# Performance work log

Hardware: AMD Instinct MI355X
Metric: run time of the kernel (lower is better)

Reference implementation:

```python
import jax, jax.numpy as jnp
import numpy as np

D_MODEL = 1024
NUM_HEADS = 16
DEPTH = D_MODEL // NUM_HEADS


def setup_inputs() -> dict:
    key = jax.random.key(0)
    ks = jax.random.split(key, 9)
    B, S = 2, 2048
    scale = 1.0 / np.sqrt(D_MODEL)
    x = jax.random.normal(ks[0], (B, S, D_MODEL), dtype=jnp.float32)
    wq = jax.random.normal(ks[1], (D_MODEL, D_MODEL), dtype=jnp.float32) * scale
    wk = jax.random.normal(ks[2], (D_MODEL, D_MODEL), dtype=jnp.float32) * scale
    wv = jax.random.normal(ks[3], (D_MODEL, D_MODEL), dtype=jnp.float32) * scale
    wo = jax.random.normal(ks[4], (D_MODEL, D_MODEL), dtype=jnp.float32) * scale
    bq = jnp.zeros((D_MODEL,), dtype=jnp.float32)
    bk = jnp.zeros((D_MODEL,), dtype=jnp.float32)
    bv = jnp.zeros((D_MODEL,), dtype=jnp.float32)
    bo = jnp.zeros((D_MODEL,), dtype=jnp.float32)
    return {"x": x, "wq": wq, "bq": bq, "wk": wk, "bk": bk,
            "wv": wv, "bv": bv, "wo": wo, "bo": bo}


def _split_heads(t):
    # [B, S, D] -> [B, H, S, depth]
    B, S, _ = t.shape
    return t.reshape(B, S, NUM_HEADS, DEPTH).transpose(0, 2, 1, 3)


def reference(x, wq, bq, wk, bk, wv, bv, wo, bo):
    q = _split_heads(x @ wq + bq)
    k = _split_heads(x @ wk + bk)
    v = _split_heads(x @ wv + bv)
    # scaled dot-product attention with materialized [B,H,S,S] scores
    logits = jnp.einsum("bhqd,bhkd->bhqk", q, k) / jnp.sqrt(
        jnp.asarray(DEPTH, dtype=x.dtype))
    attn = jax.nn.softmax(logits, axis=-1)
    out = jnp.einsum("bhqk,bhkd->bhqd", attn, v)
    B, _, S, _ = out.shape
    concat = out.transpose(0, 2, 1, 3).reshape(B, S, D_MODEL)
    return concat @ wo + bo
```

## Files before the change

kernel.cpp:

```cpp
#include <hip/hip_runtime.h>
#include <hip/hip_bf16.h>
#include <stdint.h>

typedef unsigned short u16;
typedef __attribute__((ext_vector_type(8))) short short8;
typedef __attribute__((ext_vector_type(4))) short s4v;
typedef __attribute__((ext_vector_type(4))) float f32x4;

__device__ __forceinline__ float bf2f(u16 u) {
    union { uint32_t u; float f; } v; v.u = ((uint32_t)u) << 16; return v.f;
}
__device__ __forceinline__ u16 f2bf(float f) {
    union { float f; uint32_t u; } v; v.f = f;
    uint32_t r = (v.u + 0x7fffu + ((v.u >> 16) & 1u)) >> 16;
    return (u16)r;
}
__device__ __forceinline__ uint32_t pkbf(float a, float b) {
    union { __hip_bfloat162 h; uint32_t w; } u;
    u.h = __float22bfloat162_rn(float2{a, b});
    return u.w;
}
__device__ __forceinline__ void store_out(u16* p, float v) { *p = f2bf(v); }
__device__ __forceinline__ void store_out(float* p, float v) { *p = v; }

__device__ __forceinline__ void async_ld16(const u16* g, u16* l) {
    __builtin_amdgcn_global_load_lds(
        (const __attribute__((address_space(1))) void*)g,
        (__attribute__((address_space(3))) void*)l, 16, 0, 0);
}

__global__ void cvt_x(const float* __restrict__ x, u16* __restrict__ xb) {
    int i = (blockIdx.x * 256 + threadIdx.x) * 8;
    float4 a = *(const float4*)(x + i);
    float4 b = *(const float4*)(x + i + 4);
    union { uint32_t w[4]; uint4 v; } o;
    o.w[0] = pkbf(a.x, a.y); o.w[1] = pkbf(a.z, a.w);
    o.w[2] = pkbf(b.x, b.y); o.w[3] = pkbf(b.z, b.w);
    *(uint4*)(xb + i) = o.v;
}

__global__ void transpose3(const float* __restrict__ w0, const float* __restrict__ w1,
                           const float* __restrict__ w2, u16* __restrict__ out) {
    const int z = blockIdx.z;
    const float* in = (z == 0) ? w0 : (z == 1) ? w1 : w2;
    u16* o = out + (size_t)z * 1024 * 1024;
    __shared__ u16 tile[32][33];
    int x = blockIdx.x * 32 + threadIdx.x;
    int y0 = blockIdx.y * 32;
#pragma unroll
    for (int j = threadIdx.y; j < 32; j += 8)
        tile[j][threadIdx.x] = f2bf(in[(size_t)(y0 + j) * 1024 + x]);
    __syncthreads();
    int ox = blockIdx.y * 32 + threadIdx.x;
    int oy0 = blockIdx.x * 32;
#pragma unroll
    for (int j = threadIdx.y; j < 32; j += 8)
        o[(size_t)(oy0 + j) * 1024 + ox] = tile[threadIdx.x][j];
}

#define GBM 128
#define GBN 128
#define GBK 32

template <typename OutT>
__global__ __launch_bounds__(256) void gemm_bt(
    const u16* __restrict__ A, int lda,
    const u16* __restrict__ BT, int ldb,
    const float* __restrict__ bias0, const float* __restrict__ bias1,
    const float* __restrict__ bias2,
    OutT* __restrict__ C, int ldc, int K) {
    __shared__ __align__(16) u16 As[GBM * GBK];
    __shared__ __align__(16) u16 Bs[GBN * GBK];

    const int tid = threadIdx.x;
    const int wave = tid >> 6, lane = tid & 63;
    const int quad = lane >> 4, l16 = lane & 15;
    const int wr = wave >> 1, wc = wave & 1;
    const int m0 = blockIdx.y * GBM, n0 = blockIdx.x * GBN;

    const int seg = n0 >> 10;
    const float* bsel = (seg == 0) ? bias0 : (seg == 1) ? bias1 : bias2;

    f32x4 acc[4][4] = {};

    const int srow = tid >> 2;
    const int scol = (tid & 3) * 8;
    const u16* Ag0 = A + (size_t)(m0 + srow) * lda + scol;
    const u16* Ag1 = Ag0 + (size_t)64 * lda;
    const u16* Bg0 = BT + (size_t)(n0 + srow) * ldb + scol;
    const u16* Bg1 = Bg0 + (size_t)64 * ldb;
    u16* As0 = As + (wave << 9);
    u16* As1 = As0 + 64 * GBK;
    u16* Bs0 = Bs + (wave << 9);
    u16* Bs1 = Bs0 + 64 * GBK;

    for (int kb = 0; kb < K; kb += GBK) {
        async_ld16(Ag0 + kb, As0);
        async_ld16(Ag1 + kb, As1);
        async_ld16(Bg0 + kb, Bs0);
        async_ld16(Bg1 + kb, Bs1);
        __syncthreads();

        short8 af[4], bf[4];
#pragma unroll
        for (int mt = 0; mt < 4; mt++)
            af[mt] = *(const short8*)(As + (wr * 64 + mt * 16 + l16) * GBK + quad * 8);
#pragma unroll
        for (int nt = 0; nt < 4; nt++)
            bf[nt] = *(const short8*)(Bs + (wc * 64 + nt * 16 + l16) * GBK + quad * 8);
#pragma unroll
        for (int mt = 0; mt < 4; mt++)
#pragma unroll
            for (int nt = 0; nt < 4; nt++)
                acc[mt][nt] = __builtin_amdgcn_mfma_f32_16x16x32_bf16(
                    af[mt], bf[nt], acc[mt][nt], 0, 0, 0);
        __syncthreads();
    }

#pragma unroll
    for (int nt = 0; nt < 4; nt++) {
        int col = n0 + wc * 64 + nt * 16 + l16;
        float bv = bsel[col & 1023];
#pragma unroll
        for (int mt = 0; mt < 4; mt++) {
            int row = m0 + wr * 64 + mt * 16 + quad * 4;
#pragma unroll
            for (int r = 0; r < 4; r++)
                store_out(&C[(size_t)(row + r) * ldc + col], acc[mt][nt][r] + bv);
        }
    }
}

#define SEQ 2048
#define BQ 64
#define BKV 128
#define LDK 72
#define LDKV 136

__global__ __launch_bounds__(256) void attn(u16* __restrict__ QKV) {
    __shared__ __align__(16) u16 Ks[BKV * LDK];
    __shared__ __align__(16) u16 Vs[64 * LDKV];

    const int tid = threadIdx.x;
    const int wave = tid >> 6, lane = tid & 63;
    const int quad = lane >> 4, l16 = lane & 15;
    const int h = blockIdx.y, bb = blockIdx.z;
    const int q0 = blockIdx.x * BQ;
    const size_t tok0 = (size_t)bb * SEQ;

    const u16* Qb = QKV + tok0 * 3072 + h * 64;
    const u16* Kb = QKV + tok0 * 3072 + 1024 + h * 64;
    const u16* Vb = QKV + tok0 * 3072 + 2048 + h * 64;

    const float cs = 0.18033688011112042f;

    const int qrow = q0 + wave * 16 + l16;
    short8 aq[2];
    {
        union { short8 s; u16 u[8]; uint32_t w[4]; } qa, qb;
        qa.s = *(const short8*)(Qb + (size_t)qrow * 3072 + quad * 8);
        qb.s = *(const short8*)(Qb + (size_t)qrow * 3072 + 32 + quad * 8);
#pragma unroll
        for (int j = 0; j < 4; j++) {
            qa.w[j] = pkbf(bf2f(qa.u[2 * j]) * cs, bf2f(qa.u[2 * j + 1]) * cs);
            qb.w[j] = pkbf(bf2f(qb.u[2 * j]) * cs, bf2f(qb.u[2 * j + 1]) * cs);
        }
        aq[0] = qa.s; aq[1] = qb.s;
    }

    float l_i = 0.0f;
    f32x4 o[4] = {};

    const int srow = tid >> 2;
    const int scc = (tid & 3) * 16;
    const int pr = tid & 63;
    const int dg = wave;

    const u16* kg = Kb + (size_t)srow * 3072 + scc;
    const u16* vg = Vb + (size_t)(2 * pr) * 3072 + dg * 16;

    uint4 k0r = *(const uint4*)(kg);
    uint4 k1r = *(const uint4*)(kg + 8);
    uint4 k2r = *(const uint4*)(kg + (size_t)64 * 3072);
    uint4 k3r = *(const uint4*)(kg + (size_t)64 * 3072 + 8);
    uint4 va0 = *(const uint4*)(vg);
    uint4 va1 = *(const uint4*)(vg + 8);
    uint4 vb0 = *(const uint4*)(vg + 3072);
    uint4 vb1 = *(const uint4*)(vg + 3072 + 8);

    for (int j0 = 0; j0 < SEQ; j0 += BKV) {
        *(uint4*)(Ks + srow * LDK + scc) = k0r;
        *(uint4*)(Ks + srow * LDK + scc + 8) = k1r;
        *(uint4*)(Ks + (srow + 64) * LDK + scc) = k2r;
        *(uint4*)(Ks + (srow + 64) * LDK + scc + 8) = k3r;
        {
            union { uint4 v[2]; u16 u[16]; } a, b;
            a.v[0] = va0; a.v[1] = va1; b.v[0] = vb0; b.v[1] = vb1;
#pragma unroll
            for (int j = 0; j < 16; j++) {
                uint32_t w = (uint32_t)a.u[j] | ((uint32_t)b.u[j] << 16);
                *(uint32_t*)(Vs + (dg * 16 + j) * LDKV + 2 * pr) = w;
            }
        }
        __syncthreads();

        if (j0 + BKV < SEQ) {
            size_t off = (size_t)(j0 + BKV) * 3072;
            k0r = *(const uint4*)(kg + off);
            k1r = *(const uint4*)(kg + off + 8);
            k2r = *(const uint4*)(kg + off + (size_t)64 * 3072);
            k3r = *(const uint4*)(kg + off + (size_t)64 * 3072 + 8);
            va0 = *(const uint4*)(vg + off);
            va1 = *(const uint4*)(vg + off + 8);
            vb0 = *(const uint4*)(vg + off + 3072);
            vb1 = *(const uint4*)(vg + off + 3072 + 8);
        }

        f32x4 st[8];
#pragma unroll
        for (int kkt = 0; kkt < 8; kkt++) {
            f32x4 s = {};
#pragma unroll
            for (int k2 = 0; k2 < 2; k2++) {
                short8 ak = *(const short8*)(Ks + (kkt * 16 + l16) * LDK + k2 * 32 + quad * 8);
                s = __builtin_amdgcn_mfma_f32_16x16x32_bf16(ak, aq[k2], s, 0, 0, 0);
            }
            st[kkt] = s;
        }

#pragma unroll
        for (int kkt = 0; kkt < 8; kkt++)
#pragma unroll
            for (int r = 0; r < 4; r++)
                st[kkt][r] = __builtin_amdgcn_exp2f(st[kkt][r]);

        {
            float ls = 0.0f;
#pragma unroll
            for (int kkt = 0; kkt < 8; kkt++)
#pragma unroll
                for (int r = 0; r < 4; r++) ls += st[kkt][r];
            ls += __shfl_xor(ls, 16, 64);
            ls += __shfl_xor(ls, 32, 64);
            l_i += ls;
        }

#pragma unroll
        for (int kkt = 0; kkt < 8; kkt++) {
            union { uint32_t w[2]; s4v s; } bp;
            bp.w[0] = pkbf(st[kkt][0], st[kkt][1]);
            bp.w[1] = pkbf(st[kkt][2], st[kkt][3]);
#pragma unroll
            for (int dt = 0; dt < 4; dt++) {
                s4v av = *(const s4v*)(Vs + (dt * 16 + l16) * LDKV + kkt * 16 + quad * 4);
                o[dt] = __builtin_amdgcn_mfma_f32_16x16x16bf16_1k(av, bp.s, o[dt], 0, 0, 0);
            }
        }

        __syncthreads();
    }

    const float inv_l = 1.0f / l_i;
    u16* orow = QKV + (tok0 + qrow) * 3072 + h * 64;
#pragma unroll
    for (int dt = 0; dt < 4; dt++) {
        uint32_t w0 = pkbf(o[dt][0] * inv_l, o[dt][1] * inv_l);
        uint32_t w1 = pkbf(o[dt][2] * inv_l, o[dt][3] * inv_l);
        uint2 w = {w0, w1};
        *(uint2*)(orow + dt * 16 + quad * 4) = w;
    }
}

extern "C" void kernel_launch(void* const* d_in, const int* in_sizes, int n_in,
                              void* d_out, int out_size, void* d_ws, size_t ws_size,
                              hipStream_t stream) {
    const float* x  = (const float*)d_in[0];
    const float* wq = (const float*)d_in[1];
    const float* bq = (const float*)d_in[2];
    const float* wk = (const float*)d_in[3];
    const float* bk = (const float*)d_in[4];
    const float* wv = (const float*)d_in[5];
    const float* bv = (const float*)d_in[6];
    const float* wo = (const float*)d_in[7];
    const float* bo = (const float*)d_in[8];
    (void)in_sizes; (void)n_in; (void)out_size; (void)ws_size;

    u16* QKV = (u16*)d_ws;
    u16* wT  = QKV + (size_t)4096 * 3072;
    u16* xb  = wT + (size_t)3 * 1024 * 1024;
    u16* woT = xb;

    cvt_x<<<dim3(2048), dim3(256), 0, stream>>>(x, xb);
    transpose3<<<dim3(32, 32, 3), dim3(32, 8), 0, stream>>>(wq, wk, wv, wT);
    gemm_bt<u16><<<dim3(24, 32), 256, 0, stream>>>(xb, 1024, wT, 1024, bq, bk, bv,
                                                   QKV, 3072, 1024);
    transpose3<<<dim3(32, 32, 1), dim3(32, 8), 0, stream>>>(wo, wo, wo, woT);
    attn<<<dim3(32, 16, 2), 256, 0, stream>>>(QKV);
    gemm_bt<float><<<dim3(8, 32), 256, 0, stream>>>(QKV, 3072, woT, 1024, bo, bo, bo,
                                                    (float*)d_out, 1024, 1024);
}
```

Before: 233.1 us.

## Double query tile per attention block and fold row-sum into MFMA via ones row

```diff
diff --git a/kernel.cpp b/kernel.cpp
--- a/kernel.cpp
+++ b/kernel.cpp
@@ -132,20 +132,20 @@
 }
 
 #define SEQ 2048
-#define BQ 64
+#define BQT 128
 #define BKV 128
 #define LDK 72
 #define LDKV 136
 
-__global__ __launch_bounds__(256) void attn(u16* __restrict__ QKV) {
+__global__ __launch_bounds__(512, 4) void attn(u16* __restrict__ QKV) {
     __shared__ __align__(16) u16 Ks[BKV * LDK];
-    __shared__ __align__(16) u16 Vs[64 * LDKV];
+    __shared__ __align__(16) u16 Vs[80 * LDKV];
 
     const int tid = threadIdx.x;
     const int wave = tid >> 6, lane = tid & 63;
     const int quad = lane >> 4, l16 = lane & 15;
     const int h = blockIdx.y, bb = blockIdx.z;
-    const int q0 = blockIdx.x * BQ;
+    const int q0 = blockIdx.x * BQT;
     const size_t tok0 = (size_t)bb * SEQ;
 
     const u16* Qb = QKV + tok0 * 3072 + h * 64;
@@ -153,6 +153,9 @@
     const u16* Vb = QKV + tok0 * 3072 + 2048 + h * 64;
 
     const float cs = 0.18033688011112042f;
+
+    for (int i = tid; i < 16 * LDKV; i += 512)
+        Vs[64 * LDKV + i] = (i < LDKV) ? (u16)0x3F80 : (u16)0;
 
     const int qrow = q0 + wave * 16 + l16;
     short8 aq[2];
@@ -168,8 +171,7 @@
         aq[0] = qa.s; aq[1] = qb.s;
     }
 
-    float l_i = 0.0f;
-    f32x4 o[4] = {};
+    f32x4 o[5] = {};
 
     const int srow = tid >> 2;
     const int scc = (tid & 3) * 16;
@@ -177,29 +179,23 @@
     const int dg = wave;
 
     const u16* kg = Kb + (size_t)srow * 3072 + scc;
-    const u16* vg = Vb + (size_t)(2 * pr) * 3072 + dg * 16;
+    const u16* vg = Vb + (size_t)(2 * pr) * 3072 + dg * 8;
 
     uint4 k0r = *(const uint4*)(kg);
     uint4 k1r = *(const uint4*)(kg + 8);
-    uint4 k2r = *(const uint4*)(kg + (size_t)64 * 3072);
-    uint4 k3r = *(const uint4*)(kg + (size_t)64 * 3072 + 8);
     uint4 va0 = *(const uint4*)(vg);
-    uint4 va1 = *(const uint4*)(vg + 8);
     uint4 vb0 = *(const uint4*)(vg + 3072);
-    uint4 vb1 = *(const uint4*)(vg + 3072 + 8);
 
     for (int j0 = 0; j0 < SEQ; j0 += BKV) {
         *(uint4*)(Ks + srow * LDK + scc) = k0r;
         *(uint4*)(Ks + srow * LDK + scc + 8) = k1r;
-        *(uint4*)(Ks + (srow + 64) * LDK + scc) = k2r;
-        *(uint4*)(Ks + (srow + 64) * LDK + scc + 8) = k3r;
         {
-            union { uint4 v[2]; u16 u[16]; } a, b;
-            a.v[0] = va0; a.v[1] = va1; b.v[0] = vb0; b.v[1] = vb1;
-#pragma unroll
-            for (int j = 0; j < 16; j++) {
+            union { uint4 v; u16 u[8]; } a, b;
+            a.v = va0; b.v = vb0;
+#pragma unroll
+            for (int j = 0; j < 8; j++) {
                 uint32_t w = (uint32_t)a.u[j] | ((uint32_t)b.u[j] << 16);
-                *(uint32_t*)(Vs + (dg * 16 + j) * LDKV + 2 * pr) = w;
+                *(uint32_t*)(Vs + (dg * 8 + j) * LDKV + 2 * pr) = w;
             }
         }
         __syncthreads();
@@ -208,12 +204,8 @@
             size_t off = (size_t)(j0 + BKV) * 3072;
             k0r = *(const uint4*)(kg + off);
             k1r = *(const uint4*)(kg + off + 8);
-            k2r = *(const uint4*)(kg + off + (size_t)64 * 3072);
-            k3r = *(const uint4*)(kg + off + (size_t)64 * 3072 + 8);
             va0 = *(const uint4*)(vg + off);
-            va1 = *(const uint4*)(vg + off + 8);
             vb0 = *(const uint4*)(vg + off + 3072);
-            vb1 = *(const uint4*)(vg + off + 3072 + 8);
         }
 
         f32x4 st[8];
@@ -234,24 +226,13 @@
             for (int r = 0; r < 4; r++)
                 st[kkt][r] = __builtin_amdgcn_exp2f(st[kkt][r]);
 
-        {
-            float ls = 0.0f;
-#pragma unroll
-            for (int kkt = 0; kkt < 8; kkt++)
-#pragma unroll
-                for (int r = 0; r < 4; r++) ls += st[kkt][r];
-            ls += __shfl_xor(ls, 16, 64);
-            ls += __shfl_xor(ls, 32, 64);
-            l_i += ls;
-        }
-
 #pragma unroll
         for (int kkt = 0; kkt < 8; kkt++) {
             union { uint32_t w[2]; s4v s; } bp;
             bp.w[0] = pkbf(st[kkt][0], st[kkt][1]);
             bp.w[1] = pkbf(st[kkt][2], st[kkt][3]);
 #pragma unroll
-            for (int dt = 0; dt < 4; dt++) {
+            for (int dt = 0; dt < 5; dt++) {
                 s4v av = *(const s4v*)(Vs + (dt * 16 + l16) * LDKV + kkt * 16 + quad * 4);
                 o[dt] = __builtin_amdgcn_mfma_f32_16x16x16bf16_1k(av, bp.s, o[dt], 0, 0, 0);
             }
@@ -260,7 +241,8 @@
         __syncthreads();
     }
 
-    const float inv_l = 1.0f / l_i;
+    const float l_q = __shfl(o[4][0], l16, 64);
+    const float inv_l = 1.0f / l_q;
     u16* orow = QKV + (tok0 + qrow) * 3072 + h * 64;
 #pragma unroll
     for (int dt = 0; dt < 4; dt++) {
@@ -295,7 +277,7 @@
     gemm_bt<u16><<<dim3(24, 32), 256, 0, stream>>>(xb, 1024, wT, 1024, bq, bk, bv,
                                                    QKV, 3072, 1024);
     transpose3<<<dim3(32, 32, 1), dim3(32, 8), 0, stream>>>(wo, wo, wo, woT);
-    attn<<<dim3(32, 16, 2), 256, 0, stream>>>(QKV);
+    attn<<<dim3(16, 16, 2), 512, 0, stream>>>(QKV);
     gemm_bt<float><<<dim3(8, 32), 256, 0, stream>>>(QKV, 3072, woT, 1024, bo, bo, bo,
                                                     (float*)d_out, 1024, 1024);
 }
```

Result: faster. 226.5 us (-2.8%).
